# Kernel optimization log

Hardware: AMD Instinct MI355X
Metric: run time of the kernel (lower is better)

## Reference

```python
import jax, jax.numpy as jnp
import numpy as np

GAMMA = 1.0  # RBF kernel width (init kwarg gamma)
N_PAIRS = 8_388_608
N_LAYERS = 8


def setup_inputs() -> dict:
    key = jax.random.key(0)
    ks = jax.random.split(key, 12)
    inp = {
        "x": jax.random.normal(ks[0], (N_PAIRS, 2), dtype=jnp.float32),
        "y": jax.random.normal(ks[1], (N_PAIRS, 2), dtype=jnp.float32),
        # input layer (clip=False)
        "W0": jax.random.normal(ks[2], (2, 2), dtype=jnp.float32),
        "b0": jax.random.normal(ks[3], (2,), dtype=jnp.float32),
        "scale0": jax.random.uniform(ks[4], (2,), dtype=jnp.float32),
        "shift0": jax.random.normal(ks[5], (2,), dtype=jnp.float32),
        # hidden layers (weights/biases clipped to [-5, 5] at construction)
        "Ws": jnp.clip(jax.random.normal(ks[6], (N_LAYERS, 2, 2), dtype=jnp.float32), -5.0, 5.0),
        "bs": jnp.clip(jax.random.normal(ks[7], (N_LAYERS, 2), dtype=jnp.float32), -5.0, 5.0),
        "scales": jax.random.uniform(ks[8], (N_LAYERS, 2), dtype=jnp.float32),
        "shifts": jax.random.normal(ks[9], (N_LAYERS, 2), dtype=jnp.float32),
        # final head Linear(2, 1)
        "Wf": jax.random.normal(ks[10], (1, 2), dtype=jnp.float32),
        "bf": jax.random.normal(ks[11], (1,), dtype=jnp.float32),
    }
    return inp


def _fraud_net(z, W0, b0, scale0, shift0, Ws, bs, scales, shifts, Wf, bf):
    # input layer: tanh(Linear(2,2)) * scale + shift   (z: [N,2])
    z = jnp.tanh(z @ W0.T + b0) * scale0 + shift0

    def step(z, p):
        W, b, s, t = p
        return jnp.tanh(z @ W.T + b) * s + t, None

    z, _ = jax.lax.scan(step, z, (Ws, bs, scales, shifts))
    # final Linear(2, 1) then squeeze -> [N]
    return (z @ Wf.T + bf)[..., 0]


def reference(x, y, W0, b0, scale0, shift0, Ws, bs, scales, shifts, Wf, bf):
    diff = x - y  # [N, 2]
    rbf = jnp.exp(-GAMMA * jnp.sum(diff * diff, axis=-1))  # [N]
    fx = _fraud_net(x, W0, b0, scale0, shift0, Ws, bs, scales, shifts, Wf, bf)
    fy = _fraud_net(y, W0, b0, scale0, shift0, Ws, bs, scales, shifts, Wf, bf)
    return rbf * fx * fy  # [N]
```

## Files before the change

### kernel.cpp

```cpp
#include <hip/hip_runtime.h>
#include <math.h>

#define N_LAYERS 8
#define TAB 48
#define TABSZ (TAB * TAB)
#define LOG2E2 2.8853900817779268f
#define NLOG2E 1.4426950408889634f
#define UCLAMP 24.0f
#define BLK 512

#if __has_builtin(__builtin_amdgcn_exp2f)
__device__ __forceinline__ float exp2_fast(float x) { return __builtin_amdgcn_exp2f(x); }
#else
__device__ __forceinline__ float exp2_fast(float x) { return __expf(0.6931471805599453f * x); }
#endif


__global__ __launch_bounds__(64) void setup48(
    const float* __restrict__ W0, const float* __restrict__ b0,
    const float* __restrict__ s0, const float* __restrict__ t0,
    const float* __restrict__ Ws, const float* __restrict__ bs,
    const float* __restrict__ ss, const float* __restrict__ ts,
    const float* __restrict__ Wf, const float* __restrict__ bf,
    float* __restrict__ fp, float4* __restrict__ gt4) {
    __shared__ float fs[16];
    __shared__ float row[TAB];
    int iy = blockIdx.x;
    int tx = threadIdx.x;

    if (tx == 0) {
        fs[0] = LOG2E2 * W0[0]; fs[1] = LOG2E2 * W0[1];
        fs[2] = LOG2E2 * W0[2]; fs[3] = LOG2E2 * W0[3];
        fs[4] = LOG2E2 * b0[0]; fs[5] = LOG2E2 * b0[1];
        for (int c = 0; c < 2; ++c) {
            float s = s0[c], t = t0[c];
            float span = fmaxf(2.2f * s, 1e-5f);
            float h  = span / (float)(TAB - 1);
            float lo = t - 0.5f * span;
            float ih = (float)(TAB - 1) / span;
            fs[6 + c]  = (s + 0.5f * span) * ih;
            fs[8 + c]  = 2.0f * s * ih;
            fs[10 + c] = lo;
            fs[12 + c] = h;
        }
        if (iy == 0)
            for (int i = 0; i < 14; ++i) fp[i] = fs[i];
    }
    __syncthreads();

    if (tx < TAB) {
        float z0 = fs[10] + (float)tx * fs[12];
        float z1 = fs[11] + (float)iy * fs[13];
        for (int l = 0; l < N_LAYERS; ++l) {
            float u0 = fmaf(z0, Ws[4 * l + 0], fmaf(z1, Ws[4 * l + 1], bs[2 * l + 0]));
            float u1 = fmaf(z0, Ws[4 * l + 2], fmaf(z1, Ws[4 * l + 3], bs[2 * l + 1]));
            z0 = fmaf(tanhf(u0), ss[2 * l + 0], ts[2 * l + 0]);
            z1 = fmaf(tanhf(u1), ss[2 * l + 1], ts[2 * l + 1]);
        }
        row[tx] = fmaf(z0, Wf[0], fmaf(z1, Wf[1], bf[0]));
    }
    __syncthreads();

    if (tx < TAB) {
        int c0 = max(tx - 1, 0);
        int c2 = min(tx + 1, TAB - 1);
        int c3 = min(tx + 2, TAB - 1);
        gt4[iy * TAB + tx] = make_float4(row[c0], row[tx], row[c2], row[c3]);
    }
}

__device__ __forceinline__ void cr_w(float f, float w[4]) {
    w[0] = f * fmaf(f, fmaf(f, -0.5f, 1.0f), -0.5f);
    w[1] = fmaf(f * f, fmaf(f, 1.5f, -2.5f), 1.0f);
    w[2] = f * fmaf(f, fmaf(f, -1.5f, 2.0f), 0.5f);
    w[3] = f * f * fmaf(f, 0.5f, -0.5f);
}

__device__ __forceinline__ float interp_two(const float4* __restrict__ tab4,
                                            float ax0, float ax1, float ay0, float ay1) {
    int ixa = min(max((int)ax0, 1), TAB - 3);
    int iya = min(max((int)ax1, 1), TAB - 3);
    int ixb = min(max((int)ay0, 1), TAB - 3);
    int iyb = min(max((int)ay1, 1), TAB - 3);
    float fxa = ax0 - (float)ixa, fya = ax1 - (float)iya;
    float fxb = ay0 - (float)ixb, fyb = ay1 - (float)iyb;

    const float4* pa = tab4 + (iya - 1) * TAB + ixa;
    const float4* pb = tab4 + (iyb - 1) * TAB + ixb;
    float4 a0 = pa[0], a1 = pa[TAB], a2 = pa[2 * TAB], a3 = pa[3 * TAB];
    float4 b0 = pb[0], b1 = pb[TAB], b2 = pb[2 * TAB], b3 = pb[3 * TAB];

    float wxa[4], wya[4], wxb[4], wyb[4];
    cr_w(fxa, wxa); cr_w(fya, wya);
    cr_w(fxb, wxb); cr_w(fyb, wyb);

    float ra0 = fmaf(a0.w, wxa[3], fmaf(a0.z, wxa[2], fmaf(a0.y, wxa[1], a0.x * wxa[0])));
    float ra1 = fmaf(a1.w, wxa[3], fmaf(a1.z, wxa[2], fmaf(a1.y, wxa[1], a1.x * wxa[0])));
    float ra2 = fmaf(a2.w, wxa[3], fmaf(a2.z, wxa[2], fmaf(a2.y, wxa[1], a2.x * wxa[0])));
    float ra3 = fmaf(a3.w, wxa[3], fmaf(a3.z, wxa[2], fmaf(a3.y, wxa[1], a3.x * wxa[0])));
    float gx  = fmaf(ra3, wya[3], fmaf(ra2, wya[2], fmaf(ra1, wya[1], ra0 * wya[0])));

    float rb0 = fmaf(b0.w, wxb[3], fmaf(b0.z, wxb[2], fmaf(b0.y, wxb[1], b0.x * wxb[0])));
    float rb1 = fmaf(b1.w, wxb[3], fmaf(b1.z, wxb[2], fmaf(b1.y, wxb[1], b1.x * wxb[0])));
    float rb2 = fmaf(b2.w, wxb[3], fmaf(b2.z, wxb[2], fmaf(b2.y, wxb[1], b2.x * wxb[0])));
    float rb3 = fmaf(b3.w, wxb[3], fmaf(b3.z, wxb[2], fmaf(b3.y, wxb[1], b3.x * wxb[0])));
    float gy  = fmaf(rb3, wyb[3], fmaf(rb2, wyb[2], fmaf(rb1, wyb[1], rb0 * wyb[0])));

    return gx * gy;
}

__device__ __forceinline__ float pair_val(const float4* __restrict__ tab4,
                                          float px0, float px1, float py0, float py1,
                                          float C0, float C1, float D0, float D1) {
    float d0 = exp2_fast(fminf(px0, UCLAMP)) + 1.0f;
    float d1 = exp2_fast(fminf(px1, UCLAMP)) + 1.0f;
    float d2 = exp2_fast(fminf(py0, UCLAMP)) + 1.0f;
    float d3 = exp2_fast(fminf(py1, UCLAMP)) + 1.0f;
    float p2 = d0 * d1, p3 = p2 * d2, p4 = p3 * d3;
    float R = __builtin_amdgcn_rcpf(p4);
    float i3 = R * p3;  R *= d3;
    float i2 = R * p2;  R *= d2;
    float i1 = R * d0;
    float i0 = R * d1;
    float ux0 = fmaf(-D0, i0, C0), ux1 = fmaf(-D1, i1, C1);
    float uy0 = fmaf(-D0, i2, C0), uy1 = fmaf(-D1, i3, C1);
    return interp_two(tab4, ux0, ux1, uy0, uy1);
}

__global__ __launch_bounds__(BLK, 6) void fraud_kernel(
    const float4* __restrict__ x4, const float4* __restrict__ y4,
    const float* __restrict__ fp, const float4* __restrict__ gt4,
    float2* __restrict__ out2, int stride)
{
    __shared__ float4 tab4[TABSZ];
    for (int j = threadIdx.x; j < TABSZ; j += BLK) tab4[j] = gt4[j];
    __syncthreads();

    float Wt0 = fp[0], Wt1 = fp[1], Wt2 = fp[2], Wt3 = fp[3];
    float bt0 = fp[4], bt1 = fp[5];
    float C0 = fp[6], C1 = fp[7], D0 = fp[8], D1 = fp[9];

    int tid = blockIdx.x * BLK + threadIdx.x;
#pragma unroll
    for (int k = 0; k < 4; ++k) {
        int g = tid + k * stride;
        float4 xa = x4[g], ya = y4[g];

        float pxa0 = fmaf(xa.x, Wt0, fmaf(xa.y, Wt1, bt0));
        float pxa1 = fmaf(xa.x, Wt2, fmaf(xa.y, Wt3, bt1));
        float pya0 = fmaf(ya.x, Wt0, fmaf(ya.y, Wt1, bt0));
        float pya1 = fmaf(ya.x, Wt2, fmaf(ya.y, Wt3, bt1));
        float dxA = xa.x - ya.x, dyA = xa.y - ya.y;
        float rA = exp2_fast(-NLOG2E * fmaf(dxA, dxA, dyA * dyA));
        float resA = rA * pair_val(tab4, pxa0, pxa1, pya0, pya1, C0, C1, D0, D1);

        float pxb0 = fmaf(xa.z, Wt0, fmaf(xa.w, Wt1, bt0));
        float pxb1 = fmaf(xa.z, Wt2, fmaf(xa.w, Wt3, bt1));
        float pyb0 = fmaf(ya.z, Wt0, fmaf(ya.w, Wt1, bt0));
        float pyb1 = fmaf(ya.z, Wt2, fmaf(ya.w, Wt3, bt1));
        float dxB = xa.z - ya.z, dyB = xa.w - ya.w;
        float rB = exp2_fast(-NLOG2E * fmaf(dxB, dxB, dyB * dyB));
        float resB = rB * pair_val(tab4, pxb0, pxb1, pyb0, pyb1, C0, C1, D0, D1);

        out2[g] = make_float2(resA, resB);
    }
}

extern "C" void kernel_launch(void* const* d_in, const int* in_sizes, int n_in,
                              void* d_out, int out_size, void* d_ws, size_t ws_size,
                              hipStream_t stream) {
    const float* x  = (const float*)d_in[0];
    const float* y  = (const float*)d_in[1];
    const float* W0 = (const float*)d_in[2];
    const float* b0 = (const float*)d_in[3];
    const float* s0 = (const float*)d_in[4];
    const float* t0 = (const float*)d_in[5];
    const float* Ws = (const float*)d_in[6];
    const float* bs = (const float*)d_in[7];
    const float* ss = (const float*)d_in[8];
    const float* ts = (const float*)d_in[9];
    const float* Wf = (const float*)d_in[10];
    const float* bf = (const float*)d_in[11];
    float* out = (float*)d_out;
    float* fp  = (float*)d_ws;
    float4* gt4 = (float4*)(fp + 16);

    hipLaunchKernelGGL(setup48, dim3(TAB), dim3(64), 0, stream,
                       W0, b0, s0, t0, Ws, bs, ss, ts, Wf, bf, fp, gt4);

    int n       = out_size;
    int ngroups = n / 2;
    int threads = ngroups / 4;
    dim3 block(BLK);
    dim3 grid(threads / BLK);
    hipLaunchKernelGGL(fraud_kernel, grid, block, 0, stream,
                       (const float4*)x, (const float4*)y, fp, gt4,
                       (float2*)out, threads);
}
```

Measured before the change: 188.4 us.

## Replace 2D Catmull-Rom lookup table with direct per-point network evaluation

Drops the precomputed 48x48 bicubic table of the hidden-layer stack and instead evaluates all layers per point using exp2/rcp-based tanh with constants prefolded by a single-thread setup kernel. This removes the LDS table fill, the random LDS gathers and the interpolation arithmetic, in exchange for many more transcendental instructions per element. It also shrinks the block size to 256 and removes the occupancy hint. Accuracy becomes closer to the exact reference than the interpolated table.

Result: slower. 207.0 us (+9.9%).

```diff
diff --git a/kernel.cpp b/kernel.cpp
--- a/kernel.cpp
+++ b/kernel.cpp
@@ -2,12 +2,10 @@
 #include <math.h>
 
 #define N_LAYERS 8
-#define TAB 48
-#define TABSZ (TAB * TAB)
 #define LOG2E2 2.8853900817779268f
 #define NLOG2E 1.4426950408889634f
 #define UCLAMP 24.0f
-#define BLK 512
+#define BLK 256
 
 #if __has_builtin(__builtin_amdgcn_exp2f)
 __device__ __forceinline__ float exp2_fast(float x) { return __builtin_amdgcn_exp2f(x); }
@@ -15,152 +13,71 @@
 __device__ __forceinline__ float exp2_fast(float x) { return __expf(0.6931471805599453f * x); }
 #endif
 
-
-__global__ __launch_bounds__(64) void setup48(
+__global__ __launch_bounds__(64) void setup_meta(
     const float* __restrict__ W0, const float* __restrict__ b0,
     const float* __restrict__ s0, const float* __restrict__ t0,
     const float* __restrict__ Ws, const float* __restrict__ bs,
     const float* __restrict__ ss, const float* __restrict__ ts,
     const float* __restrict__ Wf, const float* __restrict__ bf,
-    float* __restrict__ fp, float4* __restrict__ gt4) {
-    __shared__ float fs[16];
-    __shared__ float row[TAB];
-    int iy = blockIdx.x;
-    int tx = threadIdx.x;
-
-    if (tx == 0) {
-        fs[0] = LOG2E2 * W0[0]; fs[1] = LOG2E2 * W0[1];
-        fs[2] = LOG2E2 * W0[2]; fs[3] = LOG2E2 * W0[3];
-        fs[4] = LOG2E2 * b0[0]; fs[5] = LOG2E2 * b0[1];
-        for (int c = 0; c < 2; ++c) {
-            float s = s0[c], t = t0[c];
-            float span = fmaxf(2.2f * s, 1e-5f);
-            float h  = span / (float)(TAB - 1);
-            float lo = t - 0.5f * span;
-            float ih = (float)(TAB - 1) / span;
-            fs[6 + c]  = (s + 0.5f * span) * ih;
-            fs[8 + c]  = 2.0f * s * ih;
-            fs[10 + c] = lo;
-            fs[12 + c] = h;
+    float* __restrict__ fp) {
+    if (threadIdx.x == 0 && blockIdx.x == 0) {
+        fp[0] = LOG2E2 * W0[0]; fp[1] = LOG2E2 * W0[1];
+        fp[2] = LOG2E2 * W0[2]; fp[3] = LOG2E2 * W0[3];
+        fp[4] = LOG2E2 * b0[0]; fp[5] = LOG2E2 * b0[1];
+        fp[6] = -2.0f * s0[0];  fp[7] = -2.0f * s0[1];
+        fp[8] = s0[0] + t0[0];  fp[9] = s0[1] + t0[1];
+        for (int l = 0; l < N_LAYERS; ++l) {
+            float* q = fp + 10 * (l + 1);
+            q[0] = LOG2E2 * Ws[4 * l + 0]; q[1] = LOG2E2 * Ws[4 * l + 1];
+            q[2] = LOG2E2 * Ws[4 * l + 2]; q[3] = LOG2E2 * Ws[4 * l + 3];
+            q[4] = LOG2E2 * bs[2 * l + 0]; q[5] = LOG2E2 * bs[2 * l + 1];
+            q[6] = -2.0f * ss[2 * l + 0];  q[7] = -2.0f * ss[2 * l + 1];
+            q[8] = ss[2 * l + 0] + ts[2 * l + 0];
+            q[9] = ss[2 * l + 1] + ts[2 * l + 1];
         }
-        if (iy == 0)
-            for (int i = 0; i < 14; ++i) fp[i] = fs[i];
-    }
-    __syncthreads();
-
-    if (tx < TAB) {
-        float z0 = fs[10] + (float)tx * fs[12];
-        float z1 = fs[11] + (float)iy * fs[13];
-        for (int l = 0; l < N_LAYERS; ++l) {
-            float u0 = fmaf(z0, Ws[4 * l + 0], fmaf(z1, Ws[4 * l + 1], bs[2 * l + 0]));
-            float u1 = fmaf(z0, Ws[4 * l + 2], fmaf(z1, Ws[4 * l + 3], bs[2 * l + 1]));
-            z0 = fmaf(tanhf(u0), ss[2 * l + 0], ts[2 * l + 0]);
-            z1 = fmaf(tanhf(u1), ss[2 * l + 1], ts[2 * l + 1]);
-        }
-        row[tx] = fmaf(z0, Wf[0], fmaf(z1, Wf[1], bf[0]));
-    }
-    __syncthreads();
-
-    if (tx < TAB) {
-        int c0 = max(tx - 1, 0);
-        int c2 = min(tx + 1, TAB - 1);
-        int c3 = min(tx + 2, TAB - 1);
-        gt4[iy * TAB + tx] = make_float4(row[c0], row[tx], row[c2], row[c3]);
+        fp[90] = Wf[0]; fp[91] = Wf[1]; fp[92] = bf[0];
     }
 }
 
-__device__ __forceinline__ void cr_w(float f, float w[4]) {
-    w[0] = f * fmaf(f, fmaf(f, -0.5f, 1.0f), -0.5f);
-    w[1] = fmaf(f * f, fmaf(f, 1.5f, -2.5f), 1.0f);
-    w[2] = f * fmaf(f, fmaf(f, -1.5f, 2.0f), 0.5f);
-    w[3] = f * f * fmaf(f, 0.5f, -0.5f);
+__device__ __forceinline__ float net_eval(const float* __restrict__ fp,
+                                          float z0, float z1) {
+#pragma unroll
+    for (int l = 0; l < N_LAYERS + 1; ++l) {
+        const float* q = fp + 10 * l;
+        float u0 = fmaf(z0, q[0], fmaf(z1, q[1], q[4]));
+        float u1 = fmaf(z0, q[2], fmaf(z1, q[3], q[5]));
+        float d0 = exp2_fast(fminf(u0, UCLAMP)) + 1.0f;
+        float d1 = exp2_fast(fminf(u1, UCLAMP)) + 1.0f;
+        float R  = __builtin_amdgcn_rcpf(d0 * d1);
+        float i0 = R * d1;
+        float i1 = R * d0;
+        z0 = fmaf(q[6], i0, q[8]);
+        z1 = fmaf(q[7], i1, q[9]);
+    }
+    return fmaf(z0, fp[90], fmaf(z1, fp[91], fp[92]));
 }
 
-__device__ __forceinline__ float interp_two(const float4* __restrict__ tab4,
-                                            float ax0, float ax1, float ay0, float ay1) {
-    int ixa = min(max((int)ax0, 1), TAB - 3);
-    int iya = min(max((int)ax1, 1), TAB - 3);
-    int ixb = min(max((int)ay0, 1), TAB - 3);
-    int iyb = min(max((int)ay1, 1), TAB - 3);
-    float fxa = ax0 - (float)ixa, fya = ax1 - (float)iya;
-    float fxb = ay0 - (float)ixb, fyb = ay1 - (float)iyb;
-
-    const float4* pa = tab4 + (iya - 1) * TAB + ixa;
-    const float4* pb = tab4 + (iyb - 1) * TAB + ixb;
-    float4 a0 = pa[0], a1 = pa[TAB], a2 = pa[2 * TAB], a3 = pa[3 * TAB];
-    float4 b0 = pb[0], b1 = pb[TAB], b2 = pb[2 * TAB], b3 = pb[3 * TAB];
-
-    float wxa[4], wya[4], wxb[4], wyb[4];
-    cr_w(fxa, wxa); cr_w(fya, wya);
-    cr_w(fxb, wxb); cr_w(fyb, wyb);
-
-    float ra0 = fmaf(a0.w, wxa[3], fmaf(a0.z, wxa[2], fmaf(a0.y, wxa[1], a0.x * wxa[0])));
-    float ra1 = fmaf(a1.w, wxa[3], fmaf(a1.z, wxa[2], fmaf(a1.y, wxa[1], a1.x * wxa[0])));
-    float ra2 = fmaf(a2.w, wxa[3], fmaf(a2.z, wxa[2], fmaf(a2.y, wxa[1], a2.x * wxa[0])));
-    float ra3 = fmaf(a3.w, wxa[3], fmaf(a3.z, wxa[2], fmaf(a3.y, wxa[1], a3.x * wxa[0])));
-    float gx  = fmaf(ra3, wya[3], fmaf(ra2, wya[2], fmaf(ra1, wya[1], ra0 * wya[0])));
-
-    float rb0 = fmaf(b0.w, wxb[3], fmaf(b0.z, wxb[2], fmaf(b0.y, wxb[1], b0.x * wxb[0])));
-    float rb1 = fmaf(b1.w, wxb[3], fmaf(b1.z, wxb[2], fmaf(b1.y, wxb[1], b1.x * wxb[0])));
-    float rb2 = fmaf(b2.w, wxb[3], fmaf(b2.z, wxb[2], fmaf(b2.y, wxb[1], b2.x * wxb[0])));
-    float rb3 = fmaf(b3.w, wxb[3], fmaf(b3.z, wxb[2], fmaf(b3.y, wxb[1], b3.x * wxb[0])));
-    float gy  = fmaf(rb3, wyb[3], fmaf(rb2, wyb[2], fmaf(rb1, wyb[1], rb0 * wyb[0])));
-
-    return gx * gy;
-}
-
-__device__ __forceinline__ float pair_val(const float4* __restrict__ tab4,
-                                          float px0, float px1, float py0, float py1,
-                                          float C0, float C1, float D0, float D1) {
-    float d0 = exp2_fast(fminf(px0, UCLAMP)) + 1.0f;
-    float d1 = exp2_fast(fminf(px1, UCLAMP)) + 1.0f;
-    float d2 = exp2_fast(fminf(py0, UCLAMP)) + 1.0f;
-    float d3 = exp2_fast(fminf(py1, UCLAMP)) + 1.0f;
-    float p2 = d0 * d1, p3 = p2 * d2, p4 = p3 * d3;
-    float R = __builtin_amdgcn_rcpf(p4);
-    float i3 = R * p3;  R *= d3;
-    float i2 = R * p2;  R *= d2;
-    float i1 = R * d0;
-    float i0 = R * d1;
-    float ux0 = fmaf(-D0, i0, C0), ux1 = fmaf(-D1, i1, C1);
-    float uy0 = fmaf(-D0, i2, C0), uy1 = fmaf(-D1, i3, C1);
-    return interp_two(tab4, ux0, ux1, uy0, uy1);
-}
-
-__global__ __launch_bounds__(BLK, 6) void fraud_kernel(
+__global__ __launch_bounds__(BLK) void fraud_kernel(
     const float4* __restrict__ x4, const float4* __restrict__ y4,
-    const float* __restrict__ fp, const float4* __restrict__ gt4,
-    float2* __restrict__ out2, int stride)
+    const float* __restrict__ fp, float2* __restrict__ out2, int stride)
 {
-    __shared__ float4 tab4[TABSZ];
-    for (int j = threadIdx.x; j < TABSZ; j += BLK) tab4[j] = gt4[j];
-    __syncthreads();
-
-    float Wt0 = fp[0], Wt1 = fp[1], Wt2 = fp[2], Wt3 = fp[3];
-    float bt0 = fp[4], bt1 = fp[5];
-    float C0 = fp[6], C1 = fp[7], D0 = fp[8], D1 = fp[9];
-
     int tid = blockIdx.x * BLK + threadIdx.x;
 #pragma unroll
     for (int k = 0; k < 4; ++k) {
         int g = tid + k * stride;
         float4 xa = x4[g], ya = y4[g];
 
-        float pxa0 = fmaf(xa.x, Wt0, fmaf(xa.y, Wt1, bt0));
-        float pxa1 = fmaf(xa.x, Wt2, fmaf(xa.y, Wt3, bt1));
-        float pya0 = fmaf(ya.x, Wt0, fmaf(ya.y, Wt1, bt0));
-        float pya1 = fmaf(ya.x, Wt2, fmaf(ya.y, Wt3, bt1));
+        float fxA = net_eval(fp, xa.x, xa.y);
+        float fyA = net_eval(fp, ya.x, ya.y);
         float dxA = xa.x - ya.x, dyA = xa.y - ya.y;
         float rA = exp2_fast(-NLOG2E * fmaf(dxA, dxA, dyA * dyA));
-        float resA = rA * pair_val(tab4, pxa0, pxa1, pya0, pya1, C0, C1, D0, D1);
+        float resA = rA * fxA * fyA;
 
-        float pxb0 = fmaf(xa.z, Wt0, fmaf(xa.w, Wt1, bt0));
-        float pxb1 = fmaf(xa.z, Wt2, fmaf(xa.w, Wt3, bt1));
-        float pyb0 = fmaf(ya.z, Wt0, fmaf(ya.w, Wt1, bt0));
-        float pyb1 = fmaf(ya.z, Wt2, fmaf(ya.w, Wt3, bt1));
+        float fxB = net_eval(fp, xa.z, xa.w);
+        float fyB = net_eval(fp, ya.z, ya.w);
         float dxB = xa.z - ya.z, dyB = xa.w - ya.w;
         float rB = exp2_fast(-NLOG2E * fmaf(dxB, dxB, dyB * dyB));
-        float resB = rB * pair_val(tab4, pxb0, pxb1, pyb0, pyb1, C0, C1, D0, D1);
+        float resB = rB * fxB * fyB;
 
         out2[g] = make_float2(resA, resB);
     }
@@ -183,10 +100,9 @@
     const float* bf = (const float*)d_in[11];
     float* out = (float*)d_out;
     float* fp  = (float*)d_ws;
-    float4* gt4 = (float4*)(fp + 16);
 
-    hipLaunchKernelGGL(setup48, dim3(TAB), dim3(64), 0, stream,
-                       W0, b0, s0, t0, Ws, bs, ss, ts, Wf, bf, fp, gt4);
+    hipLaunchKernelGGL(setup_meta, dim3(1), dim3(64), 0, stream,
+                       W0, b0, s0, t0, Ws, bs, ss, ts, Wf, bf, fp);
 
     int n       = out_size;
     int ngroups = n / 2;
@@ -194,6 +110,6 @@
     dim3 block(BLK);
     dim3 grid(threads / BLK);
     hipLaunchKernelGGL(fraud_kernel, grid, block, 0, stream,
-                       (const float4*)x, (const float4*)y, fp, gt4,
+                       (const float4*)x, (const float4*)y, fp,
                        (float2*)out, threads);
 }
```
